# Performance work log

Measured on AMD Instinct MI355X. Metric: run time of the kernel, lower is better.

The kernel has to match this reference:

```python
import jax, jax.numpy as jnp
import numpy as np

B, HH, WW = 8, 56, 56
N = HH * WW            # 3136 tokens
DIM, NH, SR = 512, 8, 7
HDIM = DIM // 2        # 256
LDIM = DIM - HDIM      # 256
DH = LDIM // NH        # 32
SCALE = DIM ** -0.5
EPS = 1e-5


def _dwconv(x, w):
    # depthwise 3x3, stride 1, SAME (= padding k//2): x [B,C,H,W], w [C,1,3,3]
    return jax.lax.conv_general_dilated(x, w, (1, 1), 'SAME',
                                        feature_group_count=x.shape[1],
                                        dimension_numbers=('NCHW', 'OIHW', 'NCHW'))


def _bn(x, g, b, m, v):
    # inference BatchNorm2d
    s = g * jax.lax.rsqrt(v + EPS)
    return (x - m[None, :, None, None]) * s[None, :, None, None] + b[None, :, None, None]


def _avg_pool(x, k):
    return jax.lax.reduce_window(x, 0.0, jax.lax.add, (1, 1, k, k), (1, 1, k, k), 'VALID') / (k * k)


def _max_pool(x, k):
    return jax.lax.reduce_window(x, -jnp.inf, jax.lax.max, (1, 1, k, k), (1, 1, k, k), 'VALID')


def setup_inputs() -> dict:
    key = jax.random.key(0)
    ks = jax.random.split(key, 32)
    d = {}
    d['x'] = jax.random.normal(ks[0], (B, N, DIM), jnp.float32)
    d['proj_v_w'] = jax.random.normal(ks[1], (LDIM, HDIM), jnp.float32) / np.sqrt(HDIM).astype(np.float32)
    d['conv1_w'] = jax.random.normal(ks[2], (LDIM, 1, 3, 3), jnp.float32) / 3.0
    d['conv2_w'] = jax.random.normal(ks[3], (LDIM, 1, 3, 3), jnp.float32) / 3.0
    d['conv3_w'] = jax.random.normal(ks[4], (HDIM, LDIM, 1, 1), jnp.float32) / np.sqrt(LDIM).astype(np.float32)
    d['conv3_b'] = jax.random.normal(ks[5], (HDIM,), jnp.float32) * 0.1
    d['v_conv_w'] = jax.random.normal(ks[6], (LDIM, 1, 3, 3), jnp.float32) / 3.0
    d['proj_w'] = jax.random.normal(ks[7], (DIM, DIM), jnp.float32) / np.sqrt(DIM).astype(np.float32)
    d['proj_b'] = jax.random.normal(ks[8], (DIM,), jnp.float32) * 0.1
    i = 9
    for pre, c in (('bn1', LDIM), ('bn2', LDIM), ('bn3', HDIM), ('vbn', LDIM)):
        d[pre + '_g'] = jax.random.uniform(ks[i], (c,), jnp.float32, 0.8, 1.2)
        d[pre + '_b'] = jax.random.normal(ks[i + 1], (c,), jnp.float32) * 0.1
        d[pre + '_m'] = jax.random.normal(ks[i + 2], (c,), jnp.float32) * 0.1
        d[pre + '_v'] = jax.random.uniform(ks[i + 3], (c,), jnp.float32, 0.5, 1.5)
        i += 4
    return d


def reference(x, proj_v_w, conv1_w, conv2_w, conv3_w, conv3_b, v_conv_w, proj_w, proj_b,
              bn1_g, bn1_b, bn1_m, bn1_v, bn2_g, bn2_b, bn2_m, bn2_v,
              bn3_g, bn3_b, bn3_m, bn3_v, vbn_g, vbn_b, vbn_m, vbn_v):
    x_high_in = x[..., :HDIM]                       # [B,N,HDIM]
    v = x_high_in @ proj_v_w.T                      # [B,N,LDIM]
    xh = v.reshape(B, HH, WW, LDIM).transpose(0, 3, 1, 2)   # [B,LDIM,H,W]
    xh = _bn(_dwconv(xh, conv1_w), bn1_g, bn1_b, bn1_m, bn1_v)
    q1 = _avg_pool(xh, SR)                          # [B,LDIM,8,8]
    q2 = _max_pool(xh, SR)
    xh = jax.nn.gelu(xh, approximate=False)
    xh = _bn(_dwconv(xh, conv2_w), bn2_g, bn2_b, bn2_m, bn2_v)
    k1 = _avg_pool(xh, SR)
    k2 = _max_pool(xh, SR)
    xh = jax.lax.conv_general_dilated(xh, conv3_w, (1, 1), 'SAME',
                                      dimension_numbers=('NCHW', 'OIHW', 'NCHW')) + conv3_b[None, :, None, None]
    xh = _bn(xh, bn3_g, bn3_b, bn3_m, bn3_v)
    xh = jax.nn.gelu(xh, approximate=False)
    x_high = xh.reshape(B, HDIM, N).transpose(0, 2, 1)      # [B,N,HDIM]

    hq, wq = HH // SR, WW // SR
    nq = hq * wq                                    # 64 pooled tokens

    def heads(t):                                   # [B,LDIM,hq,wq] -> [B,NH,nq,DH]
        return t.reshape(B, NH, DH, nq).transpose(0, 1, 3, 2)

    q = jnp.concatenate([heads(q1), heads(q2)], axis=-1)    # [B,NH,nq,2*DH]
    k = jnp.concatenate([heads(k1), heads(k2)], axis=-1)
    vh = v.reshape(B, N, NH, DH).transpose(0, 2, 1, 3)      # [B,NH,N,DH]

    attn = jnp.einsum('bhqd,bhkd->bhqk', q, k)              # [B,NH,nq,nq]
    attn = attn.reshape(B * NH, nq, hq, wq)
    attn = jax.image.resize(attn, (B * NH, nq, HH, WW), method='bilinear', antialias=False) * SCALE
    attn = attn.reshape(B, NH, nq, N)
    attn = jax.nn.softmax(attn, axis=-1)

    out = jnp.einsum('bhqn,bhnd->bhqd', attn, vh)           # [B,NH,nq,DH]
    out = out.reshape(B, NH, hq, wq, DH).transpose(0, 1, 4, 2, 3).reshape(B, LDIM, hq, wq)
    out = jax.image.resize(out, (B, LDIM, HH, WW), method='bilinear', antialias=False)
    out = _bn(_dwconv(out, v_conv_w), vbn_g, vbn_b, vbn_m, vbn_v)
    x_low = out.reshape(B, LDIM, N).transpose(0, 2, 1)      # [B,N,LDIM]

    y = jnp.concatenate([x_high, x_low], axis=-1) @ proj_w.T + proj_b
    return y
```

## Files before the change

kernel.cpp:

```cpp
#include <hip/hip_runtime.h>
#include <math.h>

#define BB 8
#define HH 56
#define WWD 56
#define NN 3136
#define CC 256
#define DIMM 512
#define NHEAD 8
#define NQ 64
#define EPSF 1e-5f
#define SCALEF 0.04419417382415922f

typedef __attribute__((ext_vector_type(8))) short short8;
typedef __attribute__((ext_vector_type(4))) float floatx4;

__device__ __forceinline__ float gelu_f(float x) {
    return 0.5f * x * (1.f + erff(x * 0.70710678118654752f));
}
__device__ __forceinline__ unsigned short f2bf(float f) {
    union { float f; unsigned u; } v; v.f = f;
    return (unsigned short)((v.u + 0x7fffu + ((v.u >> 16) & 1u)) >> 16);
}
__device__ __forceinline__ float bf2f(unsigned short u) {
    union { unsigned u; float f; } v; v.u = ((unsigned)u) << 16;
    return v.f;
}

__global__ __launch_bounds__(256) void cast_k(const float* __restrict__ s,
                                              unsigned short* __restrict__ d, int n) {
    int i = blockIdx.x * 256 + threadIdx.x;
    if (i < n) d[i] = f2bf(s[i]);
}

__global__ __launch_bounds__(256) void gemm_v_mfma(
    const float* __restrict__ x, const unsigned short* __restrict__ w16,
    unsigned short* __restrict__ v16) {
    __shared__ short Ws[64 * 72];
    __shared__ short Xs[128 * 72];
    int n0 = blockIdx.x * 128, c0 = blockIdx.y * 64;
    int tid = threadIdx.x;
    int lane = tid & 63, wv = tid >> 6;
    int quad = lane >> 4, l16 = lane & 15;
    floatx4 zero = {0.f, 0.f, 0.f, 0.f};
    floatx4 acc[2][4];
#pragma unroll
    for (int ni = 0; ni < 2; ni++)
#pragma unroll
        for (int ci = 0; ci < 4; ci++) acc[ni][ci] = zero;

    for (int k0 = 0; k0 < 256; k0 += 64) {
        {
            int m = tid >> 1;
            int ob = (tid & 1) * 4;
            const float* src = x + (size_t)(n0 + m) * DIMM + k0 + ob * 8;
            short* dst = &Xs[m * 72 + ob * 8];
#pragma unroll
            for (int i2 = 0; i2 < 4; i2++) {
                floatx4 f0 = *(const floatx4*)(src + i2 * 8);
                floatx4 f1 = *(const floatx4*)(src + i2 * 8 + 4);
                short8 pk;
                pk[0] = (short)f2bf(f0[0]); pk[1] = (short)f2bf(f0[1]);
                pk[2] = (short)f2bf(f0[2]); pk[3] = (short)f2bf(f0[3]);
                pk[4] = (short)f2bf(f1[0]); pk[5] = (short)f2bf(f1[1]);
                pk[6] = (short)f2bf(f1[2]); pk[7] = (short)f2bf(f1[3]);
                *(short8*)(dst + i2 * 8) = pk;
            }
        }
#pragma unroll
        for (int i2 = 0; i2 < 2; i2++) {
            int idx = tid + 256 * i2;
            int c = idx >> 3, o = idx & 7;
            *(short8*)&Ws[c * 72 + o * 8] =
                *(const short8*)(const short*)(w16 + (size_t)(c0 + c) * 256 + k0 + o * 8);
        }
        __syncthreads();
#pragma unroll
        for (int kc = 0; kc < 2; kc++) {
            short8 af[4], bf[2];
#pragma unroll
            for (int ci = 0; ci < 4; ci++)
                af[ci] = *(const short8*)&Ws[(ci * 16 + l16) * 72 + (kc * 4 + quad) * 8];
#pragma unroll
            for (int ni = 0; ni < 2; ni++)
                bf[ni] = *(const short8*)&Xs[(wv * 32 + ni * 16 + l16) * 72 + (kc * 4 + quad) * 8];
#pragma unroll
            for (int ni = 0; ni < 2; ni++)
#pragma unroll
                for (int ci = 0; ci < 4; ci++)
                    acc[ni][ci] = __builtin_amdgcn_mfma_f32_16x16x32_bf16(
                        af[ci], bf[ni], acc[ni][ci], 0, 0, 0);
        }
        __syncthreads();
    }
#pragma unroll
    for (int ni = 0; ni < 2; ni++) {
        int ng = n0 + wv * 32 + ni * 16 + l16;
        int b = ng / NN, n = ng - b * NN;
#pragma unroll
        for (int ci = 0; ci < 4; ci++) {
#pragma unroll
            for (int r = 0; r < 4; r++) {
                int c = c0 + ci * 16 + quad * 4 + r;
                v16[((size_t)b * CC + c) * NN + n] = f2bf(acc[ni][ci][r]);
            }
        }
    }
}

template <bool GELU>
__global__ __launch_bounds__(256) void dwconv_pool_k(
    const unsigned short* __restrict__ in, const float* __restrict__ w,
    const float* __restrict__ g, const float* __restrict__ bparm,
    const float* __restrict__ m, const float* __restrict__ v,
    unsigned short* __restrict__ out, float* __restrict__ oavg,
    float* __restrict__ omax) {
    __shared__ float Us[56 * 57];
    __shared__ float Cs[NN];
    int bc = blockIdx.x;
    int c = bc & 255;
    int tid = threadIdx.x;
    const unsigned short* ip = in + (size_t)bc * NN;
    for (int i = tid; i < NN; i += 256) {
        int y = i / 56, x = i - y * 56;
        Us[y * 57 + x] = bf2f(ip[i]);
    }
    float w0 = w[c * 9 + 0], w1 = w[c * 9 + 1], w2 = w[c * 9 + 2];
    float w3 = w[c * 9 + 3], w4 = w[c * 9 + 4], w5 = w[c * 9 + 5];
    float w6 = w[c * 9 + 6], w7 = w[c * 9 + 7], w8 = w[c * 9 + 8];
    float s = g[c] * rsqrtf(v[c] + EPSF);
    float sh = bparm[c] - m[c] * s;
    __syncthreads();
    for (int i = tid; i < NN; i += 256) {
        int y = i / 56, x = i - y * 56;
        bool ym = y > 0, yp = y < 55, xm = x > 0, xp = x < 55;
        const float* r1 = &Us[(y - 1) * 57 + x];
        const float* r2 = &Us[y * 57 + x];
        const float* r3 = &Us[(y + 1) * 57 + x];
        float acc = r2[0] * w4;
        if (xm) acc += r2[-1] * w3;
        if (xp) acc += r2[1] * w5;
        if (ym) {
            acc += r1[0] * w1;
            if (xm) acc += r1[-1] * w0;
            if (xp) acc += r1[1] * w2;
        }
        if (yp) {
            acc += r3[0] * w7;
            if (xm) acc += r3[-1] * w6;
            if (xp) acc += r3[1] * w8;
        }
        Cs[i] = acc * s + sh;
    }
    __syncthreads();
    if (tid < 64) {
        int qy = tid >> 3, qx = tid & 7;
        const float* p0 = &Cs[(qy * 7) * 56 + qx * 7];
        float sm = 0.f, mx = -INFINITY;
#pragma unroll
        for (int py = 0; py < 7; py++)
#pragma unroll
            for (int px = 0; px < 7; px++) {
                float t = p0[py * 56 + px];
                sm += t;
                mx = fmaxf(mx, t);
            }
        oavg[(size_t)bc * 64 + tid] = sm * (1.f / 49.f);
        omax[(size_t)bc * 64 + tid] = mx;
    }
    unsigned short* op = out + (size_t)bc * NN;
    for (int i = tid; i < NN; i += 256)
        op[i] = f2bf(GELU ? gelu_f(Cs[i]) : Cs[i]);
}

__global__ __launch_bounds__(256) void conv3_mfma(
    const unsigned short* __restrict__ xin, const unsigned short* __restrict__ w16,
    const float* __restrict__ bias, const float* __restrict__ g,
    const float* __restrict__ bparm, const float* __restrict__ mm,
    const float* __restrict__ vvv, unsigned short* __restrict__ out16) {
    __shared__ short As[128 * 72];
    __shared__ short Bs[64 * 72];
    int m0 = blockIdx.x * 128, c0 = blockIdx.y * 64;
    int tid = threadIdx.x;
    int lane = tid & 63, wv = tid >> 6;
    int quad = lane >> 4, l16 = lane & 15;
    int ms = tid & 127;
    int mg = m0 + ms;
    int bb = mg / NN, nn = mg - bb * NN;
    const unsigned short* arow = xin + (size_t)bb * CC * NN + nn;
    int obase = (tid >> 7) * 4;
    floatx4 zero = {0.f, 0.f, 0.f, 0.f};
    floatx4 acc[2][4];
#pragma unroll
    for (int mi = 0; mi < 2; mi++)
#pragma unroll
        for (int ci = 0; ci < 4; ci++) acc[mi][ci] = zero;

    for (int k0 = 0; k0 < 256; k0 += 64) {
#pragma unroll
        for (int ii = 0; ii < 4; ii++) {
            int o = obase + ii;
            const unsigned short* src = arow + (size_t)(k0 + o * 8) * NN;
            short8 pk;
#pragma unroll
            for (int j = 0; j < 8; j++) pk[j] = (short)src[(size_t)j * NN];
            *(short8*)&As[ms * 72 + o * 8] = pk;
        }
#pragma unroll
        for (int i2 = 0; i2 < 2; i2++) {
            int idx = tid + 256 * i2;
            int c = idx >> 3, o = idx & 7;
            *(short8*)&Bs[c * 72 + o * 8] =
                *(const short8*)(const short*)(w16 + (size_t)(c0 + c) * CC + k0 + o * 8);
        }
        __syncthreads();
#pragma unroll
        for (int kc = 0; kc < 2; kc++) {
            short8 af[2], bf[4];
#pragma unroll
            for (int mi = 0; mi < 2; mi++)
                af[mi] = *(const short8*)&As[(wv * 32 + mi * 16 + l16) * 72 + (kc * 4 + quad) * 8];
#pragma unroll
            for (int ci = 0; ci < 4; ci++)
                bf[ci] = *(const short8*)&Bs[(ci * 16 + l16) * 72 + (kc * 4 + quad) * 8];
#pragma unroll
            for (int mi = 0; mi < 2; mi++)
#pragma unroll
                for (int ci = 0; ci < 4; ci++)
                    acc[mi][ci] = __builtin_amdgcn_mfma_f32_16x16x32_bf16(
                        af[mi], bf[ci], acc[mi][ci], 0, 0, 0);
        }
        __syncthreads();
    }
#pragma unroll
    for (int ci = 0; ci < 4; ci++) {
        int co = c0 + ci * 16 + l16;
        float s = g[co] * rsqrtf(vvv[co] + EPSF);
        float sh = bparm[co] - mm[co] * s;
        float bi = bias[co];
#pragma unroll
        for (int mi = 0; mi < 2; mi++) {
            int mbase = m0 + wv * 32 + mi * 16 + quad * 4;
#pragma unroll
            for (int r = 0; r < 4; r++) {
                float val = gelu_f((acc[mi][ci][r] + bi) * s + sh);
                out16[(size_t)(mbase + r) * CC + co] = f2bf(val);
            }
        }
    }
}

__global__ __launch_bounds__(256) void attn_qk_k(
    const float* __restrict__ q1, const float* __restrict__ q2,
    const float* __restrict__ k1, const float* __restrict__ k2,
    float* __restrict__ attn_s) {
    int b = blockIdx.x >> 3, h = blockIdx.x & 7;
    __shared__ float Qs[64][64];
    __shared__ float Ks[64][64];
    int tid = threadIdx.x;
#pragma unroll
    for (int l = 0; l < 16; l++) {
        int e = tid + 256 * l;
        int dt = e >> 6, i = e & 63;
        int d = dt & 31;
        const float* sq = (dt < 32) ? q1 : q2;
        const float* sk = (dt < 32) ? k1 : k2;
        Qs[dt][i] = sq[((size_t)b * CC + h * 32 + d) * NQ + i];
        Ks[dt][i] = sk[((size_t)b * CC + h * 32 + d) * NQ + i];
    }
    __syncthreads();
    int i = tid & 63, jg = tid >> 6;
    float acc[16] = {};
    for (int dt = 0; dt < 64; dt++) {
        float qv = Qs[dt][i];
#pragma unroll
        for (int t = 0; t < 16; t++) acc[t] += qv * Ks[dt][jg * 16 + t];
    }
    float* outp = attn_s + (((size_t)(b * 8 + h) * 64 + i) * 64) + jg * 16;
#pragma unroll
    for (int t = 0; t < 16; t++) outp[t] = acc[t];
}

__global__ __launch_bounds__(256) void attn_pv_k(
    const float* __restrict__ attn_s, const unsigned short* __restrict__ v16,
    float* __restrict__ part_O, float* __restrict__ part_rs) {
    __shared__ float asub[64][68];
    __shared__ float Mq[64];
    __shared__ unsigned short Vs[32][72];
    __shared__ short po4[64][4];
    __shared__ float pw4[64][4];
    int s = blockIdx.x, bh = blockIdx.y;
    int b = bh >> 3, h = bh & 7;
    int tid = threadIdx.x;
    int lane = tid & 63, wv = tid >> 6;
    int quad = lane >> 4, l16 = lane & 15;
    {
        int q = tid & 63, jg = tid >> 6;
        const float* src = attn_s + ((size_t)bh * 64 + q) * 64 + jg * 16;
        float* dst = &asub[q][jg * 16];
#pragma unroll
        for (int t = 0; t < 4; t++) {
            floatx4 f = *(const floatx4*)(src + t * 4);
            f[0] *= SCALEF; f[1] *= SCALEF; f[2] *= SCALEF; f[3] *= SCALEF;
            *(floatx4*)(dst + t * 4) = f;
        }
    }
    __syncthreads();
    if (tid < 64) {
        float mx = asub[tid][0];
        for (int j = 1; j < 64; j++) mx = fmaxf(mx, asub[tid][j]);
        Mq[tid] = mx;
    }
    __syncthreads();
    int q = wv * 16 + l16;
    float Mv = Mq[q];
    floatx4 zero = {0.f, 0.f, 0.f, 0.f};
    floatx4 acc0 = zero, acc1 = zero;
    float rsum = 0.f;
    for (int cch = 0; cch < 7; cch++) {
        int n0 = (s * 7 + cch) * 64;
        {
            int d = tid >> 3, part = tid & 7;
            *(short8*)&Vs[d][part * 8] =
                *(const short8*)(const short*)(v16 +
                    ((size_t)(b * CC + h * 32 + d)) * NN + n0 + part * 8);
        }
        if (tid < 64) {
            int n = n0 + tid;
            int oy = n / WWD, ox = n - oy * WWD;
            float sy = (oy + 0.5f) * 0.14285714285714285f - 0.5f;
            float sx = (ox + 0.5f) * 0.14285714285714285f - 0.5f;
            float fy0 = floorf(sy), fx0 = floorf(sx);
            int y0 = (int)fy0, x0 = (int)fx0;
            float fy = sy - fy0, fx = sx - fx0;
            int y0c = max(y0, 0), y1c = min(y0 + 1, 7);
            int x0c = max(x0, 0), x1c = min(x0 + 1, 7);
            po4[tid][0] = (short)(y0c * 8 + x0c);
            po4[tid][1] = (short)(y0c * 8 + x1c);
            po4[tid][2] = (short)(y1c * 8 + x0c);
            po4[tid][3] = (short)(y1c * 8 + x1c);
            pw4[tid][0] = (1.f - fy) * (1.f - fx);
            pw4[tid][1] = (1.f - fy) * fx;
            pw4[tid][2] = fy * (1.f - fx);
            pw4[tid][3] = fy * fx;
        }
        __syncthreads();
#pragma unroll
        for (int kc = 0; kc < 2; kc++) {
            short8 af;
#pragma unroll
            for (int j = 0; j < 8; j++) {
                int np = kc * 32 + quad * 8 + j;
                float val = pw4[np][0] * asub[q][po4[np][0]]
                          + pw4[np][1] * asub[q][po4[np][1]]
                          + pw4[np][2] * asub[q][po4[np][2]]
                          + pw4[np][3] * asub[q][po4[np][3]];
                float p = exp2f((val - Mv) * 1.44269504f);
                rsum += p;
                af[j] = (short)f2bf(p);
            }
            short8 bf0 = *(const short8*)&Vs[l16][kc * 32 + quad * 8];
            short8 bf1 = *(const short8*)&Vs[16 + l16][kc * 32 + quad * 8];
            acc0 = __builtin_amdgcn_mfma_f32_16x16x32_bf16(af, bf0, acc0, 0, 0, 0);
            acc1 = __builtin_amdgcn_mfma_f32_16x16x32_bf16(af, bf1, acc1, 0, 0, 0);
        }
        __syncthreads();
    }
    rsum += __shfl_xor(rsum, 16, 64);
    rsum += __shfl_xor(rsum, 32, 64);
    size_t base = ((size_t)bh * 7 + s) * 64;
    if (lane < 16) part_rs[base + wv * 16 + lane] = rsum;
#pragma unroll
    for (int nt = 0; nt < 2; nt++) {
        floatx4 a = nt ? acc1 : acc0;
#pragma unroll
        for (int r = 0; r < 4; r++) {
            int qo = wv * 16 + quad * 4 + r;
            part_O[(base + qo) * 32 + nt * 16 + l16] = a[r];
        }
    }
}

__global__ __launch_bounds__(256) void attn_red_k(
    const float* __restrict__ part_O, const float* __restrict__ part_rs,
    float* __restrict__ out_s) {
    int idx = blockIdx.x * 256 + threadIdx.x;
    int q = idx & 63, d = (idx >> 6) & 31, bh = idx >> 11;
    float o = 0.f, rs = 0.f;
    for (int s = 0; s < 7; s++) {
        size_t base = ((size_t)bh * 7 + s) * 64;
        o += part_O[(base + q) * 32 + d];
        rs += part_rs[base + q];
    }
    int b = bh >> 3, h = bh & 7;
    out_s[((size_t)(b * CC + h * 32 + d)) * NQ + q] = o / rs;
}

__global__ __launch_bounds__(256) void upconv_k(
    const float* __restrict__ out_s, const float* __restrict__ w,
    const float* __restrict__ g, const float* __restrict__ bparm,
    const float* __restrict__ m, const float* __restrict__ v,
    unsigned short* __restrict__ xlow16) {
    __shared__ float ts[64];
    __shared__ float Us[56 * 57];
    int bc = blockIdx.x;
    int c = bc & 255;
    int tid = threadIdx.x;
    if (tid < 64) ts[tid] = out_s[(size_t)bc * 64 + tid];
    __syncthreads();
    for (int i = tid; i < NN; i += 256) {
        int y = i / 56, x = i - y * 56;
        float sy = (y + 0.5f) * 0.14285714285714285f - 0.5f;
        float sx = (x + 0.5f) * 0.14285714285714285f - 0.5f;
        float fy0 = floorf(sy), fx0 = floorf(sx);
        int y0 = (int)fy0, x0 = (int)fx0;
        float fy = sy - fy0, fx = sx - fx0;
        int y0c = max(y0, 0), y1c = min(y0 + 1, 7);
        int x0c = max(x0, 0), x1c = min(x0 + 1, 7);
        float v00 = ts[y0c * 8 + x0c], v01 = ts[y0c * 8 + x1c];
        float v10 = ts[y1c * 8 + x0c], v11 = ts[y1c * 8 + x1c];
        Us[y * 57 + x] = (1.f - fy) * ((1.f - fx) * v00 + fx * v01) +
                         fy * ((1.f - fx) * v10 + fx * v11);
    }
    float w0 = w[c * 9 + 0], w1 = w[c * 9 + 1], w2 = w[c * 9 + 2];
    float w3 = w[c * 9 + 3], w4 = w[c * 9 + 4], w5 = w[c * 9 + 5];
    float w6 = w[c * 9 + 6], w7 = w[c * 9 + 7], w8 = w[c * 9 + 8];
    float s = g[c] * rsqrtf(v[c] + EPSF);
    float sh = bparm[c] - m[c] * s;
    __syncthreads();
    unsigned short* op = xlow16 + (size_t)bc * NN;
    for (int i = tid; i < NN; i += 256) {
        int y = i / 56, x = i - y * 56;
        bool ym = y > 0, yp = y < 55, xm = x > 0, xp = x < 55;
        const float* r1 = &Us[(y - 1) * 57 + x];
        const float* r2 = &Us[y * 57 + x];
        const float* r3 = &Us[(y + 1) * 57 + x];
        float acc = r2[0] * w4;
        if (xm) acc += r2[-1] * w3;
        if (xp) acc += r2[1] * w5;
        if (ym) {
            acc += r1[0] * w1;
            if (xm) acc += r1[-1] * w0;
            if (xp) acc += r1[1] * w2;
        }
        if (yp) {
            acc += r3[0] * w7;
            if (xm) acc += r3[-1] * w6;
            if (xp) acc += r3[1] * w8;
        }
        op[i] = f2bf(acc * s + sh);
    }
}

__global__ __launch_bounds__(256) void proj_mfma(
    const unsigned short* __restrict__ xh16, const unsigned short* __restrict__ xl16,
    const unsigned short* __restrict__ w16, const float* __restrict__ bias,
    float* __restrict__ y) {
    __shared__ short As[128 * 72];
    __shared__ short Bs[64 * 72];
    int m0 = blockIdx.x * 128, c0 = blockIdx.y * 64;
    int tid = threadIdx.x;
    int lane = tid & 63, wv = tid >> 6;
    int quad = lane >> 4, l16 = lane & 15;
    int ms = tid & 127;
    int mg = m0 + ms;
    int bb = mg / NN, nn = mg - bb * NN;
    const unsigned short* lrow = xl16 + (size_t)bb * CC * NN + nn;
    int obase = (tid >> 7) * 4;
    floatx4 zero = {0.f, 0.f, 0.f, 0.f};
    floatx4 acc[2][4];
#pragma unroll
    for (int mi = 0; mi < 2; mi++)
#pragma unroll
        for (int ci = 0; ci < 4; ci++) acc[mi][ci] = zero;

    for (int k0 = 0; k0 < 512; k0 += 64) {
        if (k0 < 256) {
#pragma unroll
            for (int i2 = 0; i2 < 4; i2++) {
                int idx = tid + 256 * i2;
                int m = idx >> 3, o = idx & 7;
                *(short8*)&As[m * 72 + o * 8] =
                    *(const short8*)(const short*)(xh16 + (size_t)(m0 + m) * CC + k0 + o * 8);
            }
        } else {
#pragma unroll
            for (int ii = 0; ii < 4; ii++) {
                int o = obase + ii;
                const unsigned short* src = lrow + (size_t)(k0 - 256 + o * 8) * NN;
                short8 pk;
#pragma unroll
                for (int j = 0; j < 8; j++) pk[j] = (short)src[(size_t)j * NN];
                *(short8*)&As[ms * 72 + o * 8] = pk;
            }
        }
#pragma unroll
        for (int i2 = 0; i2 < 2; i2++) {
            int idx = tid + 256 * i2;
            int c = idx >> 3, o = idx & 7;
            *(short8*)&Bs[c * 72 + o * 8] =
                *(const short8*)(const short*)(w16 + (size_t)(c0 + c) * DIMM + k0 + o * 8);
        }
        __syncthreads();
#pragma unroll
        for (int kc = 0; kc < 2; kc++) {
            short8 af[2], bf[4];
#pragma unroll
            for (int mi = 0; mi < 2; mi++)
                af[mi] = *(const short8*)&As[(wv * 32 + mi * 16 + l16) * 72 + (kc * 4 + quad) * 8];
#pragma unroll
            for (int ci = 0; ci < 4; ci++)
                bf[ci] = *(const short8*)&Bs[(ci * 16 + l16) * 72 + (kc * 4 + quad) * 8];
#pragma unroll
            for (int mi = 0; mi < 2; mi++)
#pragma unroll
                for (int ci = 0; ci < 4; ci++)
                    acc[mi][ci] = __builtin_amdgcn_mfma_f32_16x16x32_bf16(
                        af[mi], bf[ci], acc[mi][ci], 0, 0, 0);
        }
        __syncthreads();
    }
#pragma unroll
    for (int mi = 0; mi < 2; mi++) {
        int mbase = m0 + wv * 32 + mi * 16 + quad * 4;
#pragma unroll
        for (int ci = 0; ci < 4; ci++) {
            int co = c0 + ci * 16 + l16;
            float bi = bias[co];
#pragma unroll
            for (int r = 0; r < 4; r++)
                y[(size_t)(mbase + r) * DIMM + co] = acc[mi][ci][r] + bi;
        }
    }
}

extern "C" void kernel_launch(void* const* d_in, const int* in_sizes, int n_in,
                              void* d_out, int out_size, void* d_ws, size_t ws_size,
                              hipStream_t stream) {
    const float* x        = (const float*)d_in[0];
    const float* proj_v_w = (const float*)d_in[1];
    const float* conv1_w  = (const float*)d_in[2];
    const float* conv2_w  = (const float*)d_in[3];
    const float* conv3_w  = (const float*)d_in[4];
    const float* conv3_b  = (const float*)d_in[5];
    const float* v_conv_w = (const float*)d_in[6];
    const float* proj_w   = (const float*)d_in[7];
    const float* proj_b   = (const float*)d_in[8];
    const float* bn1_g = (const float*)d_in[9],  *bn1_b = (const float*)d_in[10];
    const float* bn1_m = (const float*)d_in[11], *bn1_v = (const float*)d_in[12];
    const float* bn2_g = (const float*)d_in[13], *bn2_b = (const float*)d_in[14];
    const float* bn2_m = (const float*)d_in[15], *bn2_v = (const float*)d_in[16];
    const float* bn3_g = (const float*)d_in[17], *bn3_b = (const float*)d_in[18];
    const float* bn3_m = (const float*)d_in[19], *bn3_v = (const float*)d_in[20];
    const float* vbn_g = (const float*)d_in[21], *vbn_b = (const float*)d_in[22];
    const float* vbn_m = (const float*)d_in[23], *vbn_v = (const float*)d_in[24];

    const size_t big = (size_t)BB * CC * NN;
    unsigned short* v16    = (unsigned short*)d_ws;
    unsigned short* bufA16 = v16 + big;
    unsigned short* bufB16 = bufA16 + big;
    unsigned short* xh16   = bufB16 + big;
    unsigned short* xlow16 = xh16 + big;
    float* small = (float*)(xlow16 + big);
    float* q1 = small;
    float* q2 = q1 + (size_t)BB * CC * NQ;
    float* k1 = q2 + (size_t)BB * CC * NQ;
    float* k2 = k1 + (size_t)BB * CC * NQ;
    float* attn_s = k2 + (size_t)BB * CC * NQ;
    float* out_s  = attn_s + (size_t)BB * NHEAD * NQ * NQ;
    float* part_O = out_s + (size_t)BB * CC * NQ;
    float* part_rs = part_O + (size_t)64 * 7 * 64 * 32;
    unsigned short* w16v  = (unsigned short*)(part_rs + 64 * 7 * 64);
    unsigned short* w16c3 = w16v + 65536;
    unsigned short* w16p  = w16c3 + 65536;

    cast_k<<<256, 256, 0, stream>>>(proj_v_w, w16v, 65536);
    cast_k<<<256, 256, 0, stream>>>(conv3_w, w16c3, 65536);
    cast_k<<<1024, 256, 0, stream>>>(proj_w, w16p, 262144);

    gemm_v_mfma<<<dim3(196, 4), 256, 0, stream>>>(x, w16v, v16);
    dwconv_pool_k<true><<<BB * CC, 256, 0, stream>>>(
        v16, conv1_w, bn1_g, bn1_b, bn1_m, bn1_v, bufA16, q1, q2);
    dwconv_pool_k<false><<<BB * CC, 256, 0, stream>>>(
        bufA16, conv2_w, bn2_g, bn2_b, bn2_m, bn2_v, bufB16, k1, k2);
    conv3_mfma<<<dim3(196, 4), 256, 0, stream>>>(bufB16, w16c3, conv3_b,
                                                 bn3_g, bn3_b, bn3_m, bn3_v, xh16);
    attn_qk_k<<<64, 256, 0, stream>>>(q1, q2, k1, k2, attn_s);
    attn_pv_k<<<dim3(7, 64), 256, 0, stream>>>(attn_s, v16, part_O, part_rs);
    attn_red_k<<<512, 256, 0, stream>>>(part_O, part_rs, out_s);
    upconv_k<<<BB * CC, 256, 0, stream>>>(out_s, v_conv_w,
                                          vbn_g, vbn_b, vbn_m, vbn_v, xlow16);
    proj_mfma<<<dim3(196, 8), 256, 0, stream>>>(xh16, xlow16, w16p, proj_b, (float*)d_out);
}
```

Measured before the change: 310.2 us.

## Fuse casts and dwconv pair, fold attention reduce into upconv, enlarge GEMM tiles

Merges the three weight-cast launches into one kernel. Fuses the two depthwise conv+BN+pool stages into one kernel that keeps the intermediate GELU output in shared memory instead of writing and rereading bufA. Folds the attention partial-sum reduction into the upsample conv kernel. Widens the three MFMA GEMMs to 128x128 tiles with a 2x2 wave layout. Together these cut launches and global traffic and improve operand reuse, but the bigger tiles use more registers and produce fewer blocks.

```diff
diff --git a/kernel.cpp b/kernel.cpp
--- a/kernel.cpp
+++ b/kernel.cpp
@@ -27,27 +27,34 @@
     return v.f;
 }
 
-__global__ __launch_bounds__(256) void cast_k(const float* __restrict__ s,
-                                              unsigned short* __restrict__ d, int n) {
+__global__ __launch_bounds__(256) void cast3_k(
+    const float* __restrict__ a, const float* __restrict__ b,
+    const float* __restrict__ cc, unsigned short* __restrict__ da,
+    unsigned short* __restrict__ db, unsigned short* __restrict__ dc) {
     int i = blockIdx.x * 256 + threadIdx.x;
-    if (i < n) d[i] = f2bf(s[i]);
+    if (i < 65536) {
+        da[i] = f2bf(a[i]);
+        db[i] = f2bf(b[i]);
+    }
+    if (i < 262144) dc[i] = f2bf(cc[i]);
 }
 
 __global__ __launch_bounds__(256) void gemm_v_mfma(
     const float* __restrict__ x, const unsigned short* __restrict__ w16,
     unsigned short* __restrict__ v16) {
-    __shared__ short Ws[64 * 72];
+    __shared__ short Ws[128 * 72];
     __shared__ short Xs[128 * 72];
-    int n0 = blockIdx.x * 128, c0 = blockIdx.y * 64;
+    int n0 = blockIdx.x * 128, c0 = blockIdx.y * 128;
     int tid = threadIdx.x;
     int lane = tid & 63, wv = tid >> 6;
+    int wc = wv >> 1, wn = wv & 1;
     int quad = lane >> 4, l16 = lane & 15;
     floatx4 zero = {0.f, 0.f, 0.f, 0.f};
-    floatx4 acc[2][4];
-#pragma unroll
-    for (int ni = 0; ni < 2; ni++)
-#pragma unroll
-        for (int ci = 0; ci < 4; ci++) acc[ni][ci] = zero;
+    floatx4 acc[4][4];
+#pragma unroll
+    for (int ci = 0; ci < 4; ci++)
+#pragma unroll
+        for (int ni = 0; ni < 4; ni++) acc[ci][ni] = zero;
 
     for (int k0 = 0; k0 < 256; k0 += 64) {
         {
@@ -68,7 +75,7 @@
             }
         }
 #pragma unroll
-        for (int i2 = 0; i2 < 2; i2++) {
+        for (int i2 = 0; i2 < 4; i2++) {
             int idx = tid + 256 * i2;
             int c = idx >> 3, o = idx & 7;
             *(short8*)&Ws[c * 72 + o * 8] =
@@ -77,44 +84,73 @@
         __syncthreads();
 #pragma unroll
         for (int kc = 0; kc < 2; kc++) {
-            short8 af[4], bf[2];
+            short8 af[4], bf[4];
 #pragma unroll
             for (int ci = 0; ci < 4; ci++)
-                af[ci] = *(const short8*)&Ws[(ci * 16 + l16) * 72 + (kc * 4 + quad) * 8];
-#pragma unroll
-            for (int ni = 0; ni < 2; ni++)
-                bf[ni] = *(const short8*)&Xs[(wv * 32 + ni * 16 + l16) * 72 + (kc * 4 + quad) * 8];
-#pragma unroll
-            for (int ni = 0; ni < 2; ni++)
-#pragma unroll
-                for (int ci = 0; ci < 4; ci++)
-                    acc[ni][ci] = __builtin_amdgcn_mfma_f32_16x16x32_bf16(
-                        af[ci], bf[ni], acc[ni][ci], 0, 0, 0);
-        }
-        __syncthreads();
-    }
-#pragma unroll
-    for (int ni = 0; ni < 2; ni++) {
-        int ng = n0 + wv * 32 + ni * 16 + l16;
+                af[ci] = *(const short8*)&Ws[(wc * 64 + ci * 16 + l16) * 72 + (kc * 4 + quad) * 8];
+#pragma unroll
+            for (int ni = 0; ni < 4; ni++)
+                bf[ni] = *(const short8*)&Xs[(wn * 64 + ni * 16 + l16) * 72 + (kc * 4 + quad) * 8];
+#pragma unroll
+            for (int ci = 0; ci < 4; ci++)
+#pragma unroll
+                for (int ni = 0; ni < 4; ni++)
+                    acc[ci][ni] = __builtin_amdgcn_mfma_f32_16x16x32_bf16(
+                        af[ci], bf[ni], acc[ci][ni], 0, 0, 0);
+        }
+        __syncthreads();
+    }
+#pragma unroll
+    for (int ni = 0; ni < 4; ni++) {
+        int ng = n0 + wn * 64 + ni * 16 + l16;
         int b = ng / NN, n = ng - b * NN;
 #pragma unroll
         for (int ci = 0; ci < 4; ci++) {
 #pragma unroll
             for (int r = 0; r < 4; r++) {
-                int c = c0 + ci * 16 + quad * 4 + r;
-                v16[((size_t)b * CC + c) * NN + n] = f2bf(acc[ni][ci][r]);
-            }
-        }
-    }
-}
-
-template <bool GELU>
-__global__ __launch_bounds__(256) void dwconv_pool_k(
-    const unsigned short* __restrict__ in, const float* __restrict__ w,
-    const float* __restrict__ g, const float* __restrict__ bparm,
-    const float* __restrict__ m, const float* __restrict__ v,
-    unsigned short* __restrict__ out, float* __restrict__ oavg,
-    float* __restrict__ omax) {
+                int c = c0 + wc * 64 + ci * 16 + quad * 4 + r;
+                v16[((size_t)b * CC + c) * NN + n] = f2bf(acc[ci][ni][r]);
+            }
+        }
+    }
+}
+
+__device__ __forceinline__ float dw3x3(const float* __restrict__ Us, int i,
+                                       float w0, float w1, float w2, float w3,
+                                       float w4, float w5, float w6, float w7,
+                                       float w8) {
+    int y = i / 56, x = i - y * 56;
+    bool ym = y > 0, yp = y < 55, xm = x > 0, xp = x < 55;
+    const float* r1 = &Us[(y - 1) * 57 + x];
+    const float* r2 = &Us[y * 57 + x];
+    const float* r3 = &Us[(y + 1) * 57 + x];
+    float acc = r2[0] * w4;
+    if (xm) acc += r2[-1] * w3;
+    if (xp) acc += r2[1] * w5;
+    if (ym) {
+        acc += r1[0] * w1;
+        if (xm) acc += r1[-1] * w0;
+        if (xp) acc += r1[1] * w2;
+    }
+    if (yp) {
+        acc += r3[0] * w7;
+        if (xm) acc += r3[-1] * w6;
+        if (xp) acc += r3[1] * w8;
+    }
+    return acc;
+}
+
+__global__ __launch_bounds__(256) void dwconv2x_k(
+    const unsigned short* __restrict__ in,
+    const float* __restrict__ w1c, const float* __restrict__ g1,
+    const float* __restrict__ b1, const float* __restrict__ m1,
+    const float* __restrict__ v1,
+    const float* __restrict__ w2c, const float* __restrict__ g2,
+    const float* __restrict__ b2, const float* __restrict__ m2,
+    const float* __restrict__ v2,
+    unsigned short* __restrict__ out,
+    float* __restrict__ oavg1, float* __restrict__ omax1,
+    float* __restrict__ oavg2, float* __restrict__ omax2) {
     __shared__ float Us[56 * 57];
     __shared__ float Cs[NN];
     int bc = blockIdx.x;
@@ -125,33 +161,14 @@
         int y = i / 56, x = i - y * 56;
         Us[y * 57 + x] = bf2f(ip[i]);
     }
-    float w0 = w[c * 9 + 0], w1 = w[c * 9 + 1], w2 = w[c * 9 + 2];
-    float w3 = w[c * 9 + 3], w4 = w[c * 9 + 4], w5 = w[c * 9 + 5];
-    float w6 = w[c * 9 + 6], w7 = w[c * 9 + 7], w8 = w[c * 9 + 8];
-    float s = g[c] * rsqrtf(v[c] + EPSF);
-    float sh = bparm[c] - m[c] * s;
-    __syncthreads();
-    for (int i = tid; i < NN; i += 256) {
-        int y = i / 56, x = i - y * 56;
-        bool ym = y > 0, yp = y < 55, xm = x > 0, xp = x < 55;
-        const float* r1 = &Us[(y - 1) * 57 + x];
-        const float* r2 = &Us[y * 57 + x];
-        const float* r3 = &Us[(y + 1) * 57 + x];
-        float acc = r2[0] * w4;
-        if (xm) acc += r2[-1] * w3;
-        if (xp) acc += r2[1] * w5;
-        if (ym) {
-            acc += r1[0] * w1;
-            if (xm) acc += r1[-1] * w0;
-            if (xp) acc += r1[1] * w2;
-        }
-        if (yp) {
-            acc += r3[0] * w7;
-            if (xm) acc += r3[-1] * w6;
-            if (xp) acc += r3[1] * w8;
-        }
-        Cs[i] = acc * s + sh;
-    }
+    float w0 = w1c[c * 9 + 0], w1 = w1c[c * 9 + 1], w2 = w1c[c * 9 + 2];
+    float w3 = w1c[c * 9 + 3], w4 = w1c[c * 9 + 4], w5 = w1c[c * 9 + 5];
+    float w6 = w1c[c * 9 + 6], w7 = w1c[c * 9 + 7], w8 = w1c[c * 9 + 8];
+    float s = g1[c] * rsqrtf(v1[c] + EPSF);
+    float sh = b1[c] - m1[c] * s;
+    __syncthreads();
+    for (int i = tid; i < NN; i += 256)
+        Cs[i] = dw3x3(Us, i, w0, w1, w2, w3, w4, w5, w6, w7, w8) * s + sh;
     __syncthreads();
     if (tid < 64) {
         int qy = tid >> 3, qx = tid & 7;
@@ -165,12 +182,41 @@
                 sm += t;
                 mx = fmaxf(mx, t);
             }
-        oavg[(size_t)bc * 64 + tid] = sm * (1.f / 49.f);
-        omax[(size_t)bc * 64 + tid] = mx;
-    }
+        oavg1[(size_t)bc * 64 + tid] = sm * (1.f / 49.f);
+        omax1[(size_t)bc * 64 + tid] = mx;
+    }
+    for (int i = tid; i < NN; i += 256) {
+        int y = i / 56, x = i - y * 56;
+        Us[y * 57 + x] = gelu_f(Cs[i]);
+    }
+    w0 = w2c[c * 9 + 0]; w1 = w2c[c * 9 + 1]; w2 = w2c[c * 9 + 2];
+    w3 = w2c[c * 9 + 3]; w4 = w2c[c * 9 + 4]; w5 = w2c[c * 9 + 5];
+    w6 = w2c[c * 9 + 6]; w7 = w2c[c * 9 + 7]; w8 = w2c[c * 9 + 8];
+    s = g2[c] * rsqrtf(v2[c] + EPSF);
+    sh = b2[c] - m2[c] * s;
+    __syncthreads();
     unsigned short* op = out + (size_t)bc * NN;
-    for (int i = tid; i < NN; i += 256)
-        op[i] = f2bf(GELU ? gelu_f(Cs[i]) : Cs[i]);
+    for (int i = tid; i < NN; i += 256) {
+        float val = dw3x3(Us, i, w0, w1, w2, w3, w4, w5, w6, w7, w8) * s + sh;
+        Cs[i] = val;
+        op[i] = f2bf(val);
+    }
+    __syncthreads();
+    if (tid < 64) {
+        int qy = tid >> 3, qx = tid & 7;
+        const float* p0 = &Cs[(qy * 7) * 56 + qx * 7];
+        float sm = 0.f, mx = -INFINITY;
+#pragma unroll
+        for (int py = 0; py < 7; py++)
+#pragma unroll
+            for (int px = 0; px < 7; px++) {
+                float t = p0[py * 56 + px];
+                sm += t;
+                mx = fmaxf(mx, t);
+            }
+        oavg2[(size_t)bc * 64 + tid] = sm * (1.f / 49.f);
+        omax2[(size_t)bc * 64 + tid] = mx;
+    }
 }
 
 __global__ __launch_bounds__(256) void conv3_mfma(
@@ -179,10 +225,11 @@
     const float* __restrict__ bparm, const float* __restrict__ mm,
     const float* __restrict__ vvv, unsigned short* __restrict__ out16) {
     __shared__ short As[128 * 72];
-    __shared__ short Bs[64 * 72];
-    int m0 = blockIdx.x * 128, c0 = blockIdx.y * 64;
+    __shared__ short Bs[128 * 72];
+    int m0 = blockIdx.x * 128, c0 = blockIdx.y * 128;
     int tid = threadIdx.x;
     int lane = tid & 63, wv = tid >> 6;
+    int wm = wv >> 1, wc = wv & 1;
     int quad = lane >> 4, l16 = lane & 15;
     int ms = tid & 127;
     int mg = m0 + ms;
@@ -190,9 +237,9 @@
     const unsigned short* arow = xin + (size_t)bb * CC * NN + nn;
     int obase = (tid >> 7) * 4;
     floatx4 zero = {0.f, 0.f, 0.f, 0.f};
-    floatx4 acc[2][4];
-#pragma unroll
-    for (int mi = 0; mi < 2; mi++)
+    floatx4 acc[4][4];
+#pragma unroll
+    for (int mi = 0; mi < 4; mi++)
 #pragma unroll
         for (int ci = 0; ci < 4; ci++) acc[mi][ci] = zero;
 
@@ -207,7 +254,7 @@
             *(short8*)&As[ms * 72 + o * 8] = pk;
         }
 #pragma unroll
-        for (int i2 = 0; i2 < 2; i2++) {
+        for (int i2 = 0; i2 < 4; i2++) {
             int idx = tid + 256 * i2;
             int c = idx >> 3, o = idx & 7;
             *(short8*)&Bs[c * 72 + o * 8] =
@@ -216,15 +263,15 @@
         __syncthreads();
 #pragma unroll
         for (int kc = 0; kc < 2; kc++) {
-            short8 af[2], bf[4];
-#pragma unroll
-            for (int mi = 0; mi < 2; mi++)
-                af[mi] = *(const short8*)&As[(wv * 32 + mi * 16 + l16) * 72 + (kc * 4 + quad) * 8];
+            short8 af[4], bf[4];
+#pragma unroll
+            for (int mi = 0; mi < 4; mi++)
+                af[mi] = *(const short8*)&As[(wm * 64 + mi * 16 + l16) * 72 + (kc * 4 + quad) * 8];
 #pragma unroll
             for (int ci = 0; ci < 4; ci++)
-                bf[ci] = *(const short8*)&Bs[(ci * 16 + l16) * 72 + (kc * 4 + quad) * 8];
-#pragma unroll
-            for (int mi = 0; mi < 2; mi++)
+                bf[ci] = *(const short8*)&Bs[(wc * 64 + ci * 16 + l16) * 72 + (kc * 4 + quad) * 8];
+#pragma unroll
+            for (int mi = 0; mi < 4; mi++)
 #pragma unroll
                 for (int ci = 0; ci < 4; ci++)
                     acc[mi][ci] = __builtin_amdgcn_mfma_f32_16x16x32_bf16(
@@ -234,13 +281,13 @@
     }
 #pragma unroll
     for (int ci = 0; ci < 4; ci++) {
-        int co = c0 + ci * 16 + l16;
+        int co = c0 + wc * 64 + ci * 16 + l16;
         float s = g[co] * rsqrtf(vvv[co] + EPSF);
         float sh = bparm[co] - mm[co] * s;
         float bi = bias[co];
 #pragma unroll
-        for (int mi = 0; mi < 2; mi++) {
-            int mbase = m0 + wv * 32 + mi * 16 + quad * 4;
+        for (int mi = 0; mi < 4; mi++) {
+            int mbase = m0 + wm * 64 + mi * 16 + quad * 4;
 #pragma unroll
             for (int r = 0; r < 4; r++) {
                 float val = gelu_f((acc[mi][ci][r] + bi) * s + sh);
@@ -381,23 +428,9 @@
     }
 }
 
-__global__ __launch_bounds__(256) void attn_red_k(
+__global__ __launch_bounds__(256) void upconv_k(
     const float* __restrict__ part_O, const float* __restrict__ part_rs,
-    float* __restrict__ out_s) {
-    int idx = blockIdx.x * 256 + threadIdx.x;
-    int q = idx & 63, d = (idx >> 6) & 31, bh = idx >> 11;
-    float o = 0.f, rs = 0.f;
-    for (int s = 0; s < 7; s++) {
-        size_t base = ((size_t)bh * 7 + s) * 64;
-        o += part_O[(base + q) * 32 + d];
-        rs += part_rs[base + q];
-    }
-    int b = bh >> 3, h = bh & 7;
-    out_s[((size_t)(b * CC + h * 32 + d)) * NQ + q] = o / rs;
-}
-
-__global__ __launch_bounds__(256) void upconv_k(
-    const float* __restrict__ out_s, const float* __restrict__ w,
+    const float* __restrict__ w,
     const float* __restrict__ g, const float* __restrict__ bparm,
     const float* __restrict__ m, const float* __restrict__ v,
     unsigned short* __restrict__ xlow16) {
@@ -406,7 +439,17 @@
     int bc = blockIdx.x;
     int c = bc & 255;
     int tid = threadIdx.x;
-    if (tid < 64) ts[tid] = out_s[(size_t)bc * 64 + tid];
+    if (tid < 64) {
+        int h = c >> 5, d = c & 31;
+        int bh = (bc >> 8) * 8 + h;
+        float o = 0.f, rs = 0.f;
+        for (int s7 = 0; s7 < 7; s7++) {
+            size_t base = ((size_t)bh * 7 + s7) * 64 + tid;
+            o += part_O[base * 32 + d];
+            rs += part_rs[base];
+        }
+        ts[tid] = o / rs;
+    }
     __syncthreads();
     for (int i = tid; i < NN; i += 256) {
         int y = i / 56, x = i - y * 56;
@@ -429,27 +472,8 @@
     float sh = bparm[c] - m[c] * s;
     __syncthreads();
     unsigned short* op = xlow16 + (size_t)bc * NN;
-    for (int i = tid; i < NN; i += 256) {
-        int y = i / 56, x = i - y * 56;
-        bool ym = y > 0, yp = y < 55, xm = x > 0, xp = x < 55;
-        const float* r1 = &Us[(y - 1) * 57 + x];
-        const float* r2 = &Us[y * 57 + x];
-        const float* r3 = &Us[(y + 1) * 57 + x];
-        float acc = r2[0] * w4;
-        if (xm) acc += r2[-1] * w3;
-        if (xp) acc += r2[1] * w5;
-        if (ym) {
-            acc += r1[0] * w1;
-            if (xm) acc += r1[-1] * w0;
-            if (xp) acc += r1[1] * w2;
-        }
-        if (yp) {
-            acc += r3[0] * w7;
-            if (xm) acc += r3[-1] * w6;
-            if (xp) acc += r3[1] * w8;
-        }
-        op[i] = f2bf(acc * s + sh);
-    }
+    for (int i = tid; i < NN; i += 256)
+        op[i] = f2bf(dw3x3(Us, i, w0, w1, w2, w3, w4, w5, w6, w7, w8) * s + sh);
 }
 
 __global__ __launch_bounds__(256) void proj_mfma(
@@ -457,10 +481,11 @@
     const unsigned short* __restrict__ w16, const float* __restrict__ bias,
     float* __restrict__ y) {
     __shared__ short As[128 * 72];
-    __shared__ short Bs[64 * 72];
-    int m0 = blockIdx.x * 128, c0 = blockIdx.y * 64;
+    __shared__ short Bs[128 * 72];
+    int m0 = blockIdx.x * 128, c0 = blockIdx.y * 128;
     int tid = threadIdx.x;
     int lane = tid & 63, wv = tid >> 6;
+    int wm = wv >> 1, wc = wv & 1;
     int quad = lane >> 4, l16 = lane & 15;
     int ms = tid & 127;
     int mg = m0 + ms;
@@ -468,9 +493,9 @@
     const unsigned short* lrow = xl16 + (size_t)bb * CC * NN + nn;
     int obase = (tid >> 7) * 4;
     floatx4 zero = {0.f, 0.f, 0.f, 0.f};
-    floatx4 acc[2][4];
-#pragma unroll
-    for (int mi = 0; mi < 2; mi++)
+    floatx4 acc[4][4];
+#pragma unroll
+    for (int mi = 0; mi < 4; mi++)
 #pragma unroll
         for (int ci = 0; ci < 4; ci++) acc[mi][ci] = zero;
 
@@ -495,7 +520,7 @@
             }
         }
 #pragma unroll
-        for (int i2 = 0; i2 < 2; i2++) {
+        for (int i2 = 0; i2 < 4; i2++) {
             int idx = tid + 256 * i2;
             int c = idx >> 3, o = idx & 7;
             *(short8*)&Bs[c * 72 + o * 8] =
@@ -504,15 +529,15 @@
         __syncthreads();
 #pragma unroll
         for (int kc = 0; kc < 2; kc++) {
-            short8 af[2], bf[4];
-#pragma unroll
-            for (int mi = 0; mi < 2; mi++)
-                af[mi] = *(const short8*)&As[(wv * 32 + mi * 16 + l16) * 72 + (kc * 4 + quad) * 8];
+            short8 af[4], bf[4];
+#pragma unroll
+            for (int mi = 0; mi < 4; mi++)
+                af[mi] = *(const short8*)&As[(wm * 64 + mi * 16 + l16) * 72 + (kc * 4 + quad) * 8];
 #pragma unroll
             for (int ci = 0; ci < 4; ci++)
-                bf[ci] = *(const short8*)&Bs[(ci * 16 + l16) * 72 + (kc * 4 + quad) * 8];
-#pragma unroll
-            for (int mi = 0; mi < 2; mi++)
+                bf[ci] = *(const short8*)&Bs[(wc * 64 + ci * 16 + l16) * 72 + (kc * 4 + quad) * 8];
+#pragma unroll
+            for (int mi = 0; mi < 4; mi++)
 #pragma unroll
                 for (int ci = 0; ci < 4; ci++)
                     acc[mi][ci] = __builtin_amdgcn_mfma_f32_16x16x32_bf16(
@@ -521,11 +546,11 @@
         __syncthreads();
     }
 #pragma unroll
-    for (int mi = 0; mi < 2; mi++) {
-        int mbase = m0 + wv * 32 + mi * 16 + quad * 4;
+    for (int mi = 0; mi < 4; mi++) {
+        int mbase = m0 + wm * 64 + mi * 16 + quad * 4;
 #pragma unroll
         for (int ci = 0; ci < 4; ci++) {
-            int co = c0 + ci * 16 + l16;
+            int co = c0 + wc * 64 + ci * 16 + l16;
             float bi = bias[co];
 #pragma unroll
             for (int r = 0; r < 4; r++)
@@ -574,21 +599,17 @@
     unsigned short* w16c3 = w16v + 65536;
     unsigned short* w16p  = w16c3 + 65536;
 
-    cast_k<<<256, 256, 0, stream>>>(proj_v_w, w16v, 65536);
-    cast_k<<<256, 256, 0, stream>>>(conv3_w, w16c3, 65536);
-    cast_k<<<1024, 256, 0, stream>>>(proj_w, w16p, 262144);
-
-    gemm_v_mfma<<<dim3(196, 4), 256, 0, stream>>>(x, w16v, v16);
-    dwconv_pool_k<true><<<BB * CC, 256, 0, stream>>>(
-        v16, conv1_w, bn1_g, bn1_b, bn1_m, bn1_v, bufA16, q1, q2);
-    dwconv_pool_k<false><<<BB * CC, 256, 0, stream>>>(
-        bufA16, conv2_w, bn2_g, bn2_b, bn2_m, bn2_v, bufB16, k1, k2);
-    conv3_mfma<<<dim3(196, 4), 256, 0, stream>>>(bufB16, w16c3, conv3_b,
+    cast3_k<<<1024, 256, 0, stream>>>(proj_v_w, conv3_w, proj_w, w16v, w16c3, w16p);
+
+    gemm_v_mfma<<<dim3(196, 2), 256, 0, stream>>>(x, w16v, v16);
+    dwconv2x_k<<<BB * CC, 256, 0, stream>>>(
+        v16, conv1_w, bn1_g, bn1_b, bn1_m, bn1_v,
+        conv2_w, bn2_g, bn2_b, bn2_m, bn2_v, bufB16, q1, q2, k1, k2);
+    conv3_mfma<<<dim3(196, 2), 256, 0, stream>>>(bufB16, w16c3, conv3_b,
                                                  bn3_g, bn3_b, bn3_m, bn3_v, xh16);
     attn_qk_k<<<64, 256, 0, stream>>>(q1, q2, k1, k2, attn_s);
     attn_pv_k<<<dim3(7, 64), 256, 0, stream>>>(attn_s, v16, part_O, part_rs);
-    attn_red_k<<<512, 256, 0, stream>>>(part_O, part_rs, out_s);
-    upconv_k<<<BB * CC, 256, 0, stream>>>(out_s, v_conv_w,
+    upconv_k<<<BB * CC, 256, 0, stream>>>(part_O, part_rs, v_conv_w,
                                           vbn_g, vbn_b, vbn_m, vbn_v, xlow16);
-    proj_mfma<<<dim3(196, 8), 256, 0, stream>>>(xh16, xlow16, w16p, proj_b, (float*)d_out);
-}
+    proj_mfma<<<dim3(196, 4), 256, 0, stream>>>(xh16, xlow16, w16p, proj_b, (float*)d_out);
+}
```

Result: faster. 284.5 us (-8.3%).
